# Performance work log

Hardware: AMD Instinct MI355X
Metric: run time of the kernel (lower is better)

Reference implementation:

```python
import jax, jax.numpy as jnp
import numpy as np


def setup_inputs() -> dict:
    key = jax.random.key(0)
    ks = jax.random.split(key, 6)
    B, Nab, Nag, d, K = 16, 16384, 16384, 128, 10
    return {
        "H1": jax.random.normal(ks[0], (B, Nab, d), jnp.float32),
        "H2": jax.random.normal(ks[1], (B, Nag, d), jnp.float32),
        "X1": jax.random.normal(ks[2], (B, Nab, 3), jnp.float32),
        "X2": jax.random.normal(ks[3], (B, Nag, 3), jnp.float32),
        "W1": jax.random.uniform(ks[4], (K, d, d), jnp.float32),
        "W2": jax.random.uniform(ks[5], (K, d, d), jnp.float32),
    }


def _kabsch(P, Q):
    # Rigid alignment: find R (3x3), t (3,) s.t. P @ R + t ~= Q (least squares).
    c1 = P.mean(axis=0)
    c2 = Q.mean(axis=0)
    Pc = P - c1
    Qc = Q - c2
    Hm = Pc.T @ Qc  # [3,3] covariance
    U, S, Vt = jnp.linalg.svd(Hm, full_matrices=False)
    sign = jnp.sign(jnp.linalg.det(U @ Vt))
    Dm = jnp.diag(jnp.concatenate([jnp.ones(2, dtype=P.dtype), sign[None]]))
    R = U @ Dm @ Vt
    t = c2 - c1 @ R
    return P @ R + t, R, t


def reference(H1, H2, X1, X2, W1, W2):
    # Keypoint cross-attention. Faithful to torch:
    #   alpha_1k = softmax( (H1 @ W1_k @ H2.T).mean(dim=1) / sqrt(d) )
    # Using mean-over-columns identity: (H1 @ W @ H2.T).mean(1) = H1 @ W @ mean(H2,0)
    d = H1.shape[-1]
    scale = 1.0 / np.sqrt(d)
    h2bar = H2.mean(axis=1)  # [B, d]
    h1bar = H1.mean(axis=1)  # [B, d]
    v1 = jnp.einsum('kde,be->bkd', W1, h2bar)          # W1_k @ mean(H2)
    s1 = jnp.einsum('bnd,bkd->bkn', H1, v1) * scale     # [B, K, Nab]
    a1 = jax.nn.softmax(s1, axis=-1)
    Y1 = jnp.einsum('bkn,bnc->bkc', a1, X1)             # [B, K, 3]
    v2 = jnp.einsum('kde,be->bkd', W2, h1bar)
    s2 = jnp.einsum('bmd,bkd->bkm', H2, v2) * scale     # [B, K, Nag]
    a2 = jax.nn.softmax(s2, axis=-1)
    Y2 = jnp.einsum('bkm,bmc->bkc', a2, X2)             # [B, K, 3]
    Y1_aligned, R, t = jax.vmap(_kabsch)(Y1, Y2)
    return jnp.stack([Y1, Y2, Y1_aligned], axis=1)      # [B, 3, K, 3]
```

## Files before the change

### kernel.cpp

```cpp
#include <hip/hip_runtime.h>
#include <math.h>

#define NB 16
#define NN 16384
#define DD 128
#define KK 10
#define NCHUNK 128
#define NTILE 128


__device__ __forceinline__ float4 f4add(float4 a, float4 b) {
    return make_float4(a.x + b.x, a.y + b.y, a.z + b.z, a.w + b.w);
}

__device__ __forceinline__ float kreduce16(const float a[KK], int l) {
    const bool h8 = (l & 8) != 0;
    const bool h4 = (l & 4) != 0;
    const bool h2 = (l & 2) != 0;
    const bool h1 = (l & 1) != 0;
    float b[8];
#pragma unroll
    for (int i = 0; i < 8; ++i) {
        float give = h8 ? a[i] : ((i < 2) ? a[i + 8] : 0.f);
        float r = __shfl_xor(give, 8);
        float keep = h8 ? ((i < 2) ? a[i + 8] : 0.f) : a[i];
        b[i] = keep + r;
    }
    float c[4];
#pragma unroll
    for (int i = 0; i < 4; ++i) {
        float give = h4 ? c[0] * 0.f + b[i] : b[i + 4];
        give = h4 ? b[i] : b[i + 4];
        float r = __shfl_xor(give, 4);
        float keep = h4 ? b[i + 4] : b[i];
        c[i] = keep + r;
    }
    float d2[2];
#pragma unroll
    for (int i = 0; i < 2; ++i) {
        float give = h2 ? c[i] : c[i + 2];
        float r = __shfl_xor(give, 2);
        float keep = h2 ? c[i + 2] : c[i];
        d2[i] = keep + r;
    }
    float give = h1 ? d2[0] : d2[1];
    float r = __shfl_xor(give, 1);
    float keep = h1 ? d2[1] : d2[0];
    return keep + r;
}

__global__ __launch_bounds__(256, 8) void k_sums(const float* __restrict__ H1,
                                                 const float* __restrict__ H2,
                                                 float* __restrict__ hpart) {
    int bi = blockIdx.x;
    int t = bi >> 11;
    int rem = bi & 2047;
    int b = rem >> 7;
    int chunk = rem & 127;
    const float4* src4 = (const float4*)((t ? H2 : H1)
                         + ((size_t)b * NN + (size_t)chunk * 128) * DD);
    int tid = threadIdx.x;
    float4 s = make_float4(0.f, 0.f, 0.f, 0.f);
#pragma unroll
    for (int o = 0; o < 2; ++o) {
        const float4* base = src4 + o * 2048;
        float4 x0 = base[0 * 256 + tid];
        float4 x1 = base[1 * 256 + tid];
        float4 x2 = base[2 * 256 + tid];
        float4 x3 = base[3 * 256 + tid];
        float4 x4 = base[4 * 256 + tid];
        float4 x5 = base[5 * 256 + tid];
        float4 x6 = base[6 * 256 + tid];
        float4 x7 = base[7 * 256 + tid];
        s = f4add(s, f4add(f4add(f4add(x0, x1), f4add(x2, x3)),
                           f4add(f4add(x4, x5), f4add(x6, x7))));
    }
    s.x += __shfl_xor(s.x, 32);
    s.y += __shfl_xor(s.y, 32);
    s.z += __shfl_xor(s.z, 32);
    s.w += __shfl_xor(s.w, 32);
    __shared__ float red[4][32][4];
    int wv = tid >> 6, lane = tid & 63;
    if (lane < 32) {
        red[wv][lane][0] = s.x; red[wv][lane][1] = s.y;
        red[wv][lane][2] = s.z; red[wv][lane][3] = s.w;
    }
    __syncthreads();
    if (tid < 32) {
        float t0 = 0.f, t1 = 0.f, t2 = 0.f, t3 = 0.f;
#pragma unroll
        for (int w = 0; w < 4; ++w) {
            t0 += red[w][tid][0]; t1 += red[w][tid][1];
            t2 += red[w][tid][2]; t3 += red[w][tid][3];
        }
        *(float4*)(hpart + ((size_t)(t * NB + b) * NCHUNK + chunk) * DD + tid * 4)
            = make_float4(t0, t1, t2, t3);
    }
}

__global__ __launch_bounds__(128) void k_v(const float* __restrict__ W1,
                                           const float* __restrict__ W2,
                                           const float* __restrict__ hpart,
                                           float* __restrict__ v) {
    int bi = blockIdx.x;
    int p = bi / 160;
    int rem = bi % 160;
    int b = rem / 10;
    int k = rem % 10;
    const float* W = (p ? W2 : W1) + (size_t)k * DD * DD;
    int srct = 1 - p;
    __shared__ __align__(16) float hs[DD];
    int tid = threadIdx.x;
    const float* hp = hpart + (size_t)(srct * NB + b) * NCHUNK * DD + tid;
    float s = 0.f;
#pragma unroll 8
    for (int c = 0; c < NCHUNK; ++c) s += hp[(size_t)c * DD];
    hs[tid] = s;
    __syncthreads();
    const float4* Wrow = (const float4*)(W + (size_t)tid * DD);
    const float4* h4p = (const float4*)hs;
    float acc = 0.f;
#pragma unroll 8
    for (int e4 = 0; e4 < 32; ++e4) {
        float4 w4 = Wrow[e4];
        float4 h4 = h4p[e4];
        acc += w4.x * h4.x + w4.y * h4.y + w4.z * h4.z + w4.w * h4.w;
    }
    const float SCALE = (float)(1.0 / (16384.0 * 11.313708498984761));
    v[((size_t)(p * NB + b) * KK + k) * DD + tid] = acc * SCALE;
}

__global__ __launch_bounds__(256) void k_scores(const float* __restrict__ H1,
                                                const float* __restrict__ H2,
                                                const float* __restrict__ X1,
                                                const float* __restrict__ X2,
                                                const float* __restrict__ v,
                                                float* __restrict__ spart) {
    int bi = blockIdx.x;
    int p = bi >> 11;
    int rem = bi & 2047;
    int b = rem >> 7;
    int tile = rem & 127;
    int row0 = tile << 7;
    const float* Hb = (p ? H2 : H1) + (size_t)b * NN * DD;
    const float* Xb = (p ? X2 : X1) + (size_t)b * NN * 3;
    const float* vp = v + (size_t)(p * NB + b) * KK * DD;

    __shared__ float4 v_s4[KK * DD / 4];
    __shared__ float red[4][40];

    int tid = threadIdx.x;
    for (int i = tid; i < KK * DD / 4; i += 256)
        v_s4[i] = ((const float4*)vp)[i];
    __syncthreads();

    int g = tid >> 4;
    int l = tid & 15;
    float kmask = (l < KK) ? 1.f : 0.f;

    float pse = 0.f, py0 = 0.f, py1 = 0.f, py2 = 0.f;

    int n0 = row0 + g * 2;
    const float* hp = Hb + (size_t)n0 * DD + (l << 2);
    float4 h00 = *(const float4*)(hp);
    float4 h01 = *(const float4*)(hp + 64);
    float4 h10 = *(const float4*)(hp + DD);
    float4 h11 = *(const float4*)(hp + DD + 64);
    float xa0 = Xb[(size_t)n0 * 3 + 0];
    float xa1 = Xb[(size_t)n0 * 3 + 1];
    float xa2 = Xb[(size_t)n0 * 3 + 2];
    float xb0 = Xb[(size_t)n0 * 3 + 3];
    float xb1 = Xb[(size_t)n0 * 3 + 4];
    float xb2 = Xb[(size_t)n0 * 3 + 5];

#pragma unroll
    for (int sweep = 0; sweep < 4; ++sweep) {
        float4 p00, p01, p10, p11;
        float qa0, qa1, qa2, qb0, qb1, qb2;
        if (sweep < 3) {
            const float* hpn = hp + (size_t)(sweep + 1) * 32 * DD;
            p00 = *(const float4*)(hpn);
            p01 = *(const float4*)(hpn + 64);
            p10 = *(const float4*)(hpn + DD);
            p11 = *(const float4*)(hpn + DD + 64);
            size_t xn = (size_t)(n0 + (sweep + 1) * 32) * 3;
            qa0 = Xb[xn + 0]; qa1 = Xb[xn + 1]; qa2 = Xb[xn + 2];
            qb0 = Xb[xn + 3]; qb1 = Xb[xn + 4]; qb2 = Xb[xn + 5];
        }
        float acc0[KK], acc1[KK];
#pragma unroll
        for (int k = 0; k < KK; ++k) {
            float4 v0 = v_s4[k * 32 + l];
            float4 v1 = v_s4[k * 32 + 16 + l];
            acc0[k] = h00.x * v0.x + h00.y * v0.y + h00.z * v0.z + h00.w * v0.w
                    + h01.x * v1.x + h01.y * v1.y + h01.z * v1.z + h01.w * v1.w;
            acc1[k] = h10.x * v0.x + h10.y * v0.y + h10.z * v0.z + h10.w * v0.w
                    + h11.x * v1.x + h11.y * v1.y + h11.z * v1.z + h11.w * v1.w;
        }
        float s0 = kreduce16(acc0, l);
        float s1 = kreduce16(acc1, l);
        float e0 = kmask * __expf(s0);
        float e1 = kmask * __expf(s1);
        pse += e0 + e1;
        py0 += e0 * xa0 + e1 * xb0;
        py1 += e0 * xa1 + e1 * xb1;
        py2 += e0 * xa2 + e1 * xb2;
        if (sweep < 3) {
            h00 = p00; h01 = p01; h10 = p10; h11 = p11;
            xa0 = qa0; xa1 = qa1; xa2 = qa2;
            xb0 = qb0; xb1 = qb1; xb2 = qb2;
        }
    }
    pse += __shfl_xor(pse, 16); pse += __shfl_xor(pse, 32);
    py0 += __shfl_xor(py0, 16); py0 += __shfl_xor(py0, 32);
    py1 += __shfl_xor(py1, 16); py1 += __shfl_xor(py1, 32);
    py2 += __shfl_xor(py2, 16); py2 += __shfl_xor(py2, 32);
    int wv = tid >> 6, lane = tid & 63;
    if (lane < KK) {
        red[wv][lane] = pse;
        red[wv][10 + lane] = py0;
        red[wv][20 + lane] = py1;
        red[wv][30 + lane] = py2;
    }
    __syncthreads();
    if (tid < 40) {
        float s = red[0][tid] + red[1][tid] + red[2][tid] + red[3][tid];
        spart[((size_t)(p * NB + b) * NTILE + tile) * 40 + tid] = s;
    }
}

__global__ __launch_bounds__(128) void k_final(const float* __restrict__ spart,
                                               float* __restrict__ out) {
    int b = blockIdx.x;
    int tid = threadIdx.x;
    __shared__ float acc[2][40];
    if (tid < 80) {
        int p = tid / 40, j = tid % 40;
        const float* sp = spart + (size_t)(p * NB + b) * NTILE * 40 + j;
        float s = 0.f;
        for (int tile = 0; tile < NTILE; ++tile) s += sp[(size_t)tile * 40];
        acc[p][j] = s;
    }
    __syncthreads();
    __shared__ float Ys[2][KK][3];
    if (tid < 2 * KK * 3) {
        int p = tid / 30;
        int r = tid % 30;
        int k = r / 3;
        int c = r % 3;
        float val = acc[p][10 + c * 10 + k] / acc[p][k];
        Ys[p][k][c] = val;
        out[((size_t)(b * 3 + p) * KK + k) * 3 + c] = val;
    }
    __syncthreads();
    if (tid == 0) {
        double P[KK][3], Q[KK][3];
        double c1[3] = {0, 0, 0}, c2[3] = {0, 0, 0};
        for (int i = 0; i < KK; ++i)
            for (int c = 0; c < 3; ++c) {
                P[i][c] = (double)Ys[0][i][c];
                Q[i][c] = (double)Ys[1][i][c];
                c1[c] += P[i][c];
                c2[c] += Q[i][c];
            }
        for (int c = 0; c < 3; ++c) { c1[c] /= KK; c2[c] /= KK; }
        double A0[3][3];
        for (int a = 0; a < 3; ++a)
            for (int c = 0; c < 3; ++c) {
                double s = 0;
                for (int i = 0; i < KK; ++i) s += (P[i][a] - c1[a]) * (Q[i][c] - c2[c]);
                A0[a][c] = s;
            }
        double Bm[3][3], V[3][3];
        for (int a = 0; a < 3; ++a)
            for (int c = 0; c < 3; ++c) { Bm[a][c] = A0[a][c]; V[a][c] = (a == c) ? 1.0 : 0.0; }
        for (int sweep = 0; sweep < 16; ++sweep)
            for (int p = 0; p < 2; ++p)
                for (int q = p + 1; q < 3; ++q) {
                    double al = 0, be = 0, ga = 0;
                    for (int r = 0; r < 3; ++r) {
                        al += Bm[r][p] * Bm[r][p];
                        be += Bm[r][q] * Bm[r][q];
                        ga += Bm[r][p] * Bm[r][q];
                    }
                    if (fabs(ga) < 1e-300) continue;
                    double zeta = (be - al) / (2.0 * ga);
                    double t = copysign(1.0, zeta) / (fabs(zeta) + sqrt(1.0 + zeta * zeta));
                    double cs = 1.0 / sqrt(1.0 + t * t);
                    double sn = cs * t;
                    for (int r = 0; r < 3; ++r) {
                        double bp = Bm[r][p], bq = Bm[r][q];
                        Bm[r][p] = cs * bp - sn * bq;
                        Bm[r][q] = sn * bp + cs * bq;
                        double vp = V[r][p], vq = V[r][q];
                        V[r][p] = cs * vp - sn * vq;
                        V[r][q] = sn * vp + cs * vq;
                    }
                }
        double sig[3];
        for (int j = 0; j < 3; ++j) {
            sig[j] = sqrt(Bm[0][j] * Bm[0][j] + Bm[1][j] * Bm[1][j] + Bm[2][j] * Bm[2][j]);
            if (sig[j] < 1e-300) sig[j] = 1e-300;
        }
        int jmin = 0;
        if (sig[1] < sig[jmin]) jmin = 1;
        if (sig[2] < sig[jmin]) jmin = 2;
        double det = A0[0][0] * (A0[1][1] * A0[2][2] - A0[1][2] * A0[2][1])
                   - A0[0][1] * (A0[1][0] * A0[2][2] - A0[1][2] * A0[2][0])
                   + A0[0][2] * (A0[1][0] * A0[2][1] - A0[1][1] * A0[2][0]);
        double sgn = (det >= 0.0) ? 1.0 : -1.0;
        double R[3][3];
        for (int a = 0; a < 3; ++a)
            for (int c = 0; c < 3; ++c) {
                double s = 0;
                for (int j = 0; j < 3; ++j) {
                    double dj = (j == jmin) ? sgn : 1.0;
                    s += dj * (Bm[a][j] / sig[j]) * V[c][j];
                }
                R[a][c] = s;
            }
        for (int i = 0; i < KK; ++i)
            for (int c = 0; c < 3; ++c) {
                double s = c2[c];
                for (int a = 0; a < 3; ++a) s += (P[i][a] - c1[a]) * R[a][c];
                out[((size_t)(b * 3 + 2) * KK + i) * 3 + c] = (float)s;
            }
    }
}

extern "C" void kernel_launch(void* const* d_in, const int* in_sizes, int n_in,
                              void* d_out, int out_size, void* d_ws, size_t ws_size,
                              hipStream_t stream) {
    const float* H1 = (const float*)d_in[0];
    const float* H2 = (const float*)d_in[1];
    const float* X1 = (const float*)d_in[2];
    const float* X2 = (const float*)d_in[3];
    const float* W1 = (const float*)d_in[4];
    const float* W2 = (const float*)d_in[5];
    float* out = (float*)d_out;
    float* ws = (float*)d_ws;
    float* hpart = ws;
    float* v     = ws + 524288;
    float* spart = ws + 565248;

    hipLaunchKernelGGL(k_sums,   dim3(4096), dim3(256), 0, stream, H1, H2, hpart);
    hipLaunchKernelGGL(k_v,      dim3(320),  dim3(128), 0, stream, W1, W2, hpart, v);
    hipLaunchKernelGGL(k_scores, dim3(4096), dim3(256), 0, stream, H1, H2, X1, X2, v, spart);
    hipLaunchKernelGGL(k_final,  dim3(16),   dim3(128), 0, stream, spart, out);
}
```

Measured before the change: 367.4 us.

## Fold H1 column sums into H1 scoring pass to skip a full H1 read

Restructures the pipeline: sum H2 first, compute v1, then score H1 while simultaneously accumulating H1 column partial sums, then compute v2 from those and score H2. This removes a separate full pass over H1 just to compute its mean, reducing global memory traffic. In exchange the stages become serialized with more launches and each scoring launch has half as many blocks, plus extra shuffle/shared-memory work in the H1 scoring kernel.

```diff
diff --git a/kernel.cpp b/kernel.cpp
--- a/kernel.cpp
+++ b/kernel.cpp
@@ -5,8 +5,7 @@
 #define NN 16384
 #define DD 128
 #define KK 10
-#define NCHUNK 128
-#define NTILE 128
+#define NT 128
 
 
 __device__ __forceinline__ float4 f4add(float4 a, float4 b) {
@@ -21,60 +20,46 @@
     float b[8];
 #pragma unroll
     for (int i = 0; i < 8; ++i) {
-        float give = h8 ? a[i] : ((i < 2) ? a[i + 8] : 0.f);
-        float r = __shfl_xor(give, 8);
-        float keep = h8 ? ((i < 2) ? a[i + 8] : 0.f) : a[i];
-        b[i] = keep + r;
+        float hi = (i < 2) ? a[i + 8] : 0.f;
+        float give = h8 ? a[i] : hi;
+        float keep = h8 ? hi : a[i];
+        b[i] = keep + __shfl_xor(give, 8);
     }
     float c[4];
 #pragma unroll
     for (int i = 0; i < 4; ++i) {
-        float give = h4 ? c[0] * 0.f + b[i] : b[i + 4];
-        give = h4 ? b[i] : b[i + 4];
-        float r = __shfl_xor(give, 4);
+        float give = h4 ? b[i] : b[i + 4];
         float keep = h4 ? b[i + 4] : b[i];
-        c[i] = keep + r;
+        c[i] = keep + __shfl_xor(give, 4);
     }
     float d2[2];
 #pragma unroll
     for (int i = 0; i < 2; ++i) {
         float give = h2 ? c[i] : c[i + 2];
-        float r = __shfl_xor(give, 2);
         float keep = h2 ? c[i + 2] : c[i];
-        d2[i] = keep + r;
+        d2[i] = keep + __shfl_xor(give, 2);
     }
     float give = h1 ? d2[0] : d2[1];
-    float r = __shfl_xor(give, 1);
     float keep = h1 ? d2[1] : d2[0];
-    return keep + r;
-}
-
-__global__ __launch_bounds__(256, 8) void k_sums(const float* __restrict__ H1,
-                                                 const float* __restrict__ H2,
-                                                 float* __restrict__ hpart) {
+    return keep + __shfl_xor(give, 1);
+}
+
+__global__ __launch_bounds__(256) void k_sum(const float* __restrict__ H,
+                                             float* __restrict__ hpart) {
     int bi = blockIdx.x;
-    int t = bi >> 11;
-    int rem = bi & 2047;
-    int b = rem >> 7;
-    int chunk = rem & 127;
-    const float4* src4 = (const float4*)((t ? H2 : H1)
-                         + ((size_t)b * NN + (size_t)chunk * 128) * DD);
+    int b = bi >> 7;
+    int chunk = bi & 127;
+    const float4* src4 = (const float4*)(H + ((size_t)b * NN + (size_t)chunk * 128) * DD);
     int tid = threadIdx.x;
-    float4 s = make_float4(0.f, 0.f, 0.f, 0.f);
-#pragma unroll
-    for (int o = 0; o < 2; ++o) {
-        const float4* base = src4 + o * 2048;
-        float4 x0 = base[0 * 256 + tid];
-        float4 x1 = base[1 * 256 + tid];
-        float4 x2 = base[2 * 256 + tid];
-        float4 x3 = base[3 * 256 + tid];
-        float4 x4 = base[4 * 256 + tid];
-        float4 x5 = base[5 * 256 + tid];
-        float4 x6 = base[6 * 256 + tid];
-        float4 x7 = base[7 * 256 + tid];
-        s = f4add(s, f4add(f4add(f4add(x0, x1), f4add(x2, x3)),
-                           f4add(f4add(x4, x5), f4add(x6, x7))));
-    }
+    float4 x[16];
+#pragma unroll
+    for (int j = 0; j < 16; ++j) x[j] = src4[j * 256 + tid];
+    float4 t0 = f4add(x[0], x[1]),   t1 = f4add(x[2], x[3]);
+    float4 t2 = f4add(x[4], x[5]),   t3 = f4add(x[6], x[7]);
+    float4 t4 = f4add(x[8], x[9]),   t5 = f4add(x[10], x[11]);
+    float4 t6 = f4add(x[12], x[13]), t7 = f4add(x[14], x[15]);
+    float4 s = f4add(f4add(f4add(t0, t1), f4add(t2, t3)),
+                     f4add(f4add(t4, t5), f4add(t6, t7)));
     s.x += __shfl_xor(s.x, 32);
     s.y += __shfl_xor(s.y, 32);
     s.z += __shfl_xor(s.z, 32);
@@ -87,37 +72,33 @@
     }
     __syncthreads();
     if (tid < 32) {
-        float t0 = 0.f, t1 = 0.f, t2 = 0.f, t3 = 0.f;
+        float t0s = 0.f, t1s = 0.f, t2s = 0.f, t3s = 0.f;
 #pragma unroll
         for (int w = 0; w < 4; ++w) {
-            t0 += red[w][tid][0]; t1 += red[w][tid][1];
-            t2 += red[w][tid][2]; t3 += red[w][tid][3];
-        }
-        *(float4*)(hpart + ((size_t)(t * NB + b) * NCHUNK + chunk) * DD + tid * 4)
-            = make_float4(t0, t1, t2, t3);
-    }
-}
-
-__global__ __launch_bounds__(128) void k_v(const float* __restrict__ W1,
-                                           const float* __restrict__ W2,
+            t0s += red[w][tid][0]; t1s += red[w][tid][1];
+            t2s += red[w][tid][2]; t3s += red[w][tid][3];
+        }
+        *(float4*)(hpart + ((size_t)b * NT + chunk) * DD + tid * 4)
+            = make_float4(t0s, t1s, t2s, t3s);
+    }
+}
+
+__global__ __launch_bounds__(128) void k_v(const float* __restrict__ W,
                                            const float* __restrict__ hpart,
-                                           float* __restrict__ v) {
+                                           float* __restrict__ vdst) {
     int bi = blockIdx.x;
-    int p = bi / 160;
-    int rem = bi % 160;
-    int b = rem / 10;
-    int k = rem % 10;
-    const float* W = (p ? W2 : W1) + (size_t)k * DD * DD;
-    int srct = 1 - p;
+    int b = bi / 10;
+    int k = bi % 10;
+    const float* Wk = W + (size_t)k * DD * DD;
     __shared__ __align__(16) float hs[DD];
     int tid = threadIdx.x;
-    const float* hp = hpart + (size_t)(srct * NB + b) * NCHUNK * DD + tid;
+    const float* hp = hpart + (size_t)b * NT * DD + tid;
     float s = 0.f;
 #pragma unroll 8
-    for (int c = 0; c < NCHUNK; ++c) s += hp[(size_t)c * DD];
+    for (int c = 0; c < NT; ++c) s += hp[(size_t)c * DD];
     hs[tid] = s;
     __syncthreads();
-    const float4* Wrow = (const float4*)(W + (size_t)tid * DD);
+    const float4* Wrow = (const float4*)(Wk + (size_t)tid * DD);
     const float4* h4p = (const float4*)hs;
     float acc = 0.f;
 #pragma unroll 8
@@ -127,27 +108,26 @@
         acc += w4.x * h4.x + w4.y * h4.y + w4.z * h4.z + w4.w * h4.w;
     }
     const float SCALE = (float)(1.0 / (16384.0 * 11.313708498984761));
-    v[((size_t)(p * NB + b) * KK + k) * DD + tid] = acc * SCALE;
-}
-
-__global__ __launch_bounds__(256) void k_scores(const float* __restrict__ H1,
-                                                const float* __restrict__ H2,
-                                                const float* __restrict__ X1,
-                                                const float* __restrict__ X2,
-                                                const float* __restrict__ v,
-                                                float* __restrict__ spart) {
+    vdst[((size_t)b * KK + k) * DD + tid] = acc * SCALE;
+}
+
+template <bool FOLD>
+__global__ __launch_bounds__(256) void k_scores(const float* __restrict__ Hsrc,
+                                                const float* __restrict__ Xsrc,
+                                                const float* __restrict__ vsrc,
+                                                float* __restrict__ spartp,
+                                                float* __restrict__ hpartdst) {
     int bi = blockIdx.x;
-    int p = bi >> 11;
-    int rem = bi & 2047;
-    int b = rem >> 7;
-    int tile = rem & 127;
+    int b = bi >> 7;
+    int tile = bi & 127;
     int row0 = tile << 7;
-    const float* Hb = (p ? H2 : H1) + (size_t)b * NN * DD;
-    const float* Xb = (p ? X2 : X1) + (size_t)b * NN * 3;
-    const float* vp = v + (size_t)(p * NB + b) * KK * DD;
+    const float* Hb = Hsrc + (size_t)b * NN * DD;
+    const float* Xb = Xsrc + (size_t)b * NN * 3;
+    const float* vp = vsrc + (size_t)b * KK * DD;
 
     __shared__ float4 v_s4[KK * DD / 4];
     __shared__ float red[4][40];
+    __shared__ float4 colred4[4][2][16];
 
     int tid = threadIdx.x;
     for (int i = tid; i < KK * DD / 4; i += 256)
@@ -159,6 +139,8 @@
     float kmask = (l < KK) ? 1.f : 0.f;
 
     float pse = 0.f, py0 = 0.f, py1 = 0.f, py2 = 0.f;
+    float4 cs0 = make_float4(0.f, 0.f, 0.f, 0.f);
+    float4 cs1 = make_float4(0.f, 0.f, 0.f, 0.f);
 
     int n0 = row0 + g * 2;
     const float* hp = Hb + (size_t)n0 * DD + (l << 2);
@@ -187,6 +169,10 @@
             qa0 = Xb[xn + 0]; qa1 = Xb[xn + 1]; qa2 = Xb[xn + 2];
             qb0 = Xb[xn + 3]; qb1 = Xb[xn + 4]; qb2 = Xb[xn + 5];
         }
+        if (FOLD) {
+            cs0 = f4add(cs0, f4add(h00, h10));
+            cs1 = f4add(cs1, f4add(h01, h11));
+        }
         float acc0[KK], acc1[KK];
 #pragma unroll
         for (int k = 0; k < KK; ++k) {
@@ -215,17 +201,40 @@
     py0 += __shfl_xor(py0, 16); py0 += __shfl_xor(py0, 32);
     py1 += __shfl_xor(py1, 16); py1 += __shfl_xor(py1, 32);
     py2 += __shfl_xor(py2, 16); py2 += __shfl_xor(py2, 32);
+    if (FOLD) {
+        cs0.x += __shfl_xor(cs0.x, 16); cs0.x += __shfl_xor(cs0.x, 32);
+        cs0.y += __shfl_xor(cs0.y, 16); cs0.y += __shfl_xor(cs0.y, 32);
+        cs0.z += __shfl_xor(cs0.z, 16); cs0.z += __shfl_xor(cs0.z, 32);
+        cs0.w += __shfl_xor(cs0.w, 16); cs0.w += __shfl_xor(cs0.w, 32);
+        cs1.x += __shfl_xor(cs1.x, 16); cs1.x += __shfl_xor(cs1.x, 32);
+        cs1.y += __shfl_xor(cs1.y, 16); cs1.y += __shfl_xor(cs1.y, 32);
+        cs1.z += __shfl_xor(cs1.z, 16); cs1.z += __shfl_xor(cs1.z, 32);
+        cs1.w += __shfl_xor(cs1.w, 16); cs1.w += __shfl_xor(cs1.w, 32);
+    }
     int wv = tid >> 6, lane = tid & 63;
-    if (lane < KK) {
-        red[wv][lane] = pse;
-        red[wv][10 + lane] = py0;
-        red[wv][20 + lane] = py1;
-        red[wv][30 + lane] = py2;
+    if (lane < 16) {
+        if (lane < KK) {
+            red[wv][lane] = pse;
+            red[wv][10 + lane] = py0;
+            red[wv][20 + lane] = py1;
+            red[wv][30 + lane] = py2;
+        }
+        if (FOLD) {
+            colred4[wv][0][lane] = cs0;
+            colred4[wv][1][lane] = cs1;
+        }
     }
     __syncthreads();
     if (tid < 40) {
         float s = red[0][tid] + red[1][tid] + red[2][tid] + red[3][tid];
-        spart[((size_t)(p * NB + b) * NTILE + tile) * 40 + tid] = s;
+        spartp[((size_t)b * NT + tile) * 40 + tid] = s;
+    }
+    if (FOLD && tid < DD) {
+        int j = tid >> 6, cc = tid & 63, ll = cc >> 2, c = cc & 3;
+        float s = 0.f;
+#pragma unroll
+        for (int w = 0; w < 4; ++w) s += ((const float*)&colred4[w][j][ll])[c];
+        hpartdst[((size_t)b * NT + tile) * DD + tid] = s;
     }
 }
 
@@ -236,9 +245,9 @@
     __shared__ float acc[2][40];
     if (tid < 80) {
         int p = tid / 40, j = tid % 40;
-        const float* sp = spart + (size_t)(p * NB + b) * NTILE * 40 + j;
+        const float* sp = spart + (size_t)(p * NB + b) * NT * 40 + j;
         float s = 0.f;
-        for (int tile = 0; tile < NTILE; ++tile) s += sp[(size_t)tile * 40];
+        for (int tile = 0; tile < NT; ++tile) s += sp[(size_t)tile * 40];
         acc[p][j] = s;
     }
     __syncthreads();
@@ -339,12 +348,20 @@
     const float* W2 = (const float*)d_in[5];
     float* out = (float*)d_out;
     float* ws = (float*)d_ws;
-    float* hpart = ws;
-    float* v     = ws + 524288;
-    float* spart = ws + 565248;
-
-    hipLaunchKernelGGL(k_sums,   dim3(4096), dim3(256), 0, stream, H1, H2, hpart);
-    hipLaunchKernelGGL(k_v,      dim3(320),  dim3(128), 0, stream, W1, W2, hpart, v);
-    hipLaunchKernelGGL(k_scores, dim3(4096), dim3(256), 0, stream, H1, H2, X1, X2, v, spart);
-    hipLaunchKernelGGL(k_final,  dim3(16),   dim3(128), 0, stream, spart, out);
-}
+    float* hpart2 = ws;
+    float* hpart1 = ws + 262144;
+    float* v1     = ws + 524288;
+    float* v2     = ws + 544768;
+    float* spart  = ws + 565248;
+    float* sp1 = spart;
+    float* sp2 = spart + (size_t)NB * NT * 40;
+
+    hipLaunchKernelGGL(k_sum,            dim3(2048), dim3(256), 0, stream, H2, hpart2);
+    hipLaunchKernelGGL(k_v,              dim3(160),  dim3(128), 0, stream, W1, hpart2, v1);
+    hipLaunchKernelGGL((k_scores<true>), dim3(2048), dim3(256), 0, stream,
+                       H1, X1, v1, sp1, hpart1);
+    hipLaunchKernelGGL(k_v,              dim3(160),  dim3(128), 0, stream, W2, hpart1, v2);
+    hipLaunchKernelGGL((k_scores<false>),dim3(2048), dim3(256), 0, stream,
+                       H2, X2, v2, sp2, (float*)nullptr);
+    hipLaunchKernelGGL(k_final,          dim3(16),   dim3(128), 0, stream, spart, out);
+}
```

Result: faster. 355.2 us (-3.3%).
